# Optimization experiments

Measured on AMD Instinct MI355X. Metric: run time of the kernel, lower is better.

Reference implementation:

```python
import math
import jax, jax.numpy as jnp
import numpy as np

SCALE = 64.0
MARGIN = 0.5
T = 0.2
COS_M = math.cos(MARGIN)
SIN_M = math.sin(MARGIN)
TH = math.cos(math.pi - MARGIN)
MM = math.sin(math.pi - MARGIN) * MARGIN
EPS = 1e-07

B, D, C = 512, 512, 100000


def setup_inputs() -> dict:
    key = jax.random.key(0)
    k1, k2, k3 = jax.random.split(key, 3)
    embedding = jax.random.normal(k1, (B, D), dtype=jnp.float32)
    # xavier_uniform for (num_classes, embed_size)
    limit = math.sqrt(6.0 / (C + D))
    weight = jax.random.uniform(k2, (C, D), dtype=jnp.float32, minval=-limit, maxval=limit)
    ground_truth = jax.random.randint(k3, (B,), 0, C, dtype=jnp.int64)
    return {"embedding": embedding, "weight": weight, "ground_truth": ground_truth}


def reference(embedding, weight, ground_truth):
    gt = ground_truth.astype(jnp.int32)
    e = embedding / jnp.linalg.norm(embedding, axis=1, keepdims=True)
    w = weight / jnp.linalg.norm(weight, axis=1, keepdims=True)
    # (B, C) cosine similarities
    cos_theta = jnp.clip(jnp.einsum('bd,cd->bc', e, w), -1.0 + EPS, 1.0 - EPS)
    pos = jnp.take_along_axis(cos_theta, gt[:, None], axis=1)  # (B, 1)
    sin_theta = jnp.sqrt(jnp.clip(1.0 - pos * pos, EPS, 1.0 - EPS))
    phi = pos * COS_M - sin_theta * SIN_M
    phi = jnp.where(pos > TH, phi, pos - MM)  # easy_margin=False branch
    # hard-example reweighting: fixed=False -> (t+1)*cos + t where cos > phi
    mask = cos_theta > phi  # phi broadcasts (B,1) -> (B,C)
    cos_theta = jnp.where(mask, (T + 1.0) * cos_theta + T, cos_theta)
    # scatter phi into the ground-truth column
    output = cos_theta.at[jnp.arange(B), gt].set(phi[:, 0])
    output = output * SCALE
    # mean cross-entropy
    logp = jax.nn.log_softmax(output, axis=1)
    loss = -jnp.mean(jnp.take_along_axis(logp, gt[:, None], axis=1))
    return loss
```

## Files before the change

kernel.cpp:

```cpp
#include <hip/hip_runtime.h>
#include <hip/hip_bf16.h>
#include <stdint.h>

typedef unsigned short u16;
typedef __attribute__((ext_vector_type(8))) short short8;
typedef __attribute__((ext_vector_type(4))) float floatx4;

#define B_   512
#define D_   512
#define C_   100000

#define SCALE_  64.0f
#define COSM_   0.8775825618903728f
#define SINM_   0.479425538604203f
#define TH_     (-0.8775825618903728f)
#define MM_     0.2397127693021015f
#define EPS_    1e-7f
#define SHIFT_  89.6f

#define BM 256
#define BN 64
#define BK 32

__device__ inline float wave_reduce_sum(float v) {
    v += __shfl_xor(v, 1);
    v += __shfl_xor(v, 2);
    v += __shfl_xor(v, 4);
    v += __shfl_xor(v, 8);
    v += __shfl_xor(v, 16);
    v += __shfl_xor(v, 32);
    return v;
}

__device__ inline u16 f2bf(float x) {
    union { float f; uint32_t u; } v; v.f = x;
    uint32_t r = v.u + 0x7fffu + ((v.u >> 16) & 1u);
    return (u16)(r >> 16);
}

__global__ __launch_bounds__(256) void norm_e_phi_kernel(
    const float* __restrict__ emb, const float* __restrict__ w_raw,
    const int* __restrict__ gt, u16* __restrict__ e_bf16,
    float* __restrict__ phi, float* __restrict__ rowsum) {
    if (threadIdx.x < 4) rowsum[blockIdx.x * 4 + threadIdx.x] = 0.0f;
    int wv = threadIdx.x >> 6;
    int lane = threadIdx.x & 63;
    int b = blockIdx.x * 4 + wv;
    const float4* rp = (const float4*)(emb + (long)b * D_);
    float4 f0 = rp[lane], f1 = rp[lane + 64];
    float sq = f0.x*f0.x + f0.y*f0.y + f0.z*f0.z + f0.w*f0.w
             + f1.x*f1.x + f1.y*f1.y + f1.z*f1.z + f1.w*f1.w;
    sq = wave_reduce_sum(sq);
    float rn = 1.0f / sqrtf(sq);
    f0.x *= rn; f0.y *= rn; f0.z *= rn; f0.w *= rn;
    f1.x *= rn; f1.y *= rn; f1.z *= rn; f1.w *= rn;
    uint2 p0, p1;
    p0.x = (uint32_t)f2bf(f0.x) | ((uint32_t)f2bf(f0.y) << 16);
    p0.y = (uint32_t)f2bf(f0.z) | ((uint32_t)f2bf(f0.w) << 16);
    p1.x = (uint32_t)f2bf(f1.x) | ((uint32_t)f2bf(f1.y) << 16);
    p1.y = (uint32_t)f2bf(f1.z) | ((uint32_t)f2bf(f1.w) << 16);
    uint2* ob = (uint2*)(e_bf16 + (long)b * D_);
    ob[lane] = p0;
    ob[lane + 64] = p1;

    int g = gt[b];
    const float4* wp = (const float4*)(w_raw + (long)g * D_);
    float4 w0 = wp[lane], w1 = wp[lane + 64];
    float dt = f0.x*w0.x + f0.y*w0.y + f0.z*w0.z + f0.w*w0.w
             + f1.x*w1.x + f1.y*w1.y + f1.z*w1.z + f1.w*w1.w;
    float wsq = w0.x*w0.x + w0.y*w0.y + w0.z*w0.z + w0.w*w0.w
              + w1.x*w1.x + w1.y*w1.y + w1.z*w1.z + w1.w*w1.w;
    dt = wave_reduce_sum(dt);
    wsq = wave_reduce_sum(wsq);
    if (lane == 0) {
        float pos = dt / sqrtf(wsq);
        pos = fminf(fmaxf(pos, -1.0f + EPS_), 1.0f - EPS_);
        float s2 = 1.0f - pos * pos;
        s2 = fminf(fmaxf(s2, EPS_), 1.0f - EPS_);
        float sin_t = sqrtf(s2);
        float ph = pos * COSM_ - sin_t * SINM_;
        ph = (pos > TH_) ? ph : (pos - MM_);
        phi[b] = ph;
    }
}

__device__ inline void cvt_store(const float4& v0, const float4& v1,
                                 u16* dst, float& sq) {
    union { u16 h[8]; uint4 q; } u;
    u.h[0] = f2bf(v0.x); u.h[1] = f2bf(v0.y);
    u.h[2] = f2bf(v0.z); u.h[3] = f2bf(v0.w);
    u.h[4] = f2bf(v1.x); u.h[5] = f2bf(v1.y);
    u.h[6] = f2bf(v1.z); u.h[7] = f2bf(v1.w);
    *(uint4*)dst = u.q;
    sq += v0.x*v0.x + v0.y*v0.y + v0.z*v0.z + v0.w*v0.w
        + v1.x*v1.x + v1.y*v1.y + v1.z*v1.z + v1.w*v1.w;
}

__global__ __launch_bounds__(256, 3) void gemm_arcface_fused(
    const u16* __restrict__ a_g,
    const float* __restrict__ w_g,
    const float* __restrict__ phi, const int* __restrict__ gt,
    float* __restrict__ rowsum) {
    __shared__ __align__(16) u16 b_tile[2][BN * BK];
    __shared__ float phi_s[BM];
    __shared__ int gt_s[BM];
    __shared__ float rnorm_s[BN];

    int tid = threadIdx.x;
    int c0 = (blockIdx.x >> 1) * BN;
    int m0 = (blockIdx.x & 1) * BM;

    phi_s[tid] = phi[m0 + tid];
    gt_s[tid] = gt[m0 + tid];

    int rb = tid >> 2;
    int bslot = tid & 3;
    int bkq = bslot ^ ((rb >> 1) & 3);
    long brow_g = min(c0 + rb, C_ - 1);
    const float4* b_src = (const float4*)(w_g + brow_g * (long)D_ + bkq * 8);
    u16* b_dst0 = &b_tile[0][rb * BK + bslot * 8];
    u16* b_dst1 = &b_tile[1][rb * BK + bslot * 8];

    int wv = tid >> 6, lane = tid & 63;
    int low4 = lane & 15, quad = lane >> 4;
    int lslot = quad ^ ((low4 >> 1) & 3);
    const u16* a_base = a_g + (long)(m0 + wv * 64 + low4) * D_ + quad * 8;
    int bf_off = low4 * BK + lslot * 8;

    floatx4 acc[4][4] = {};
    float sq = 0.0f;
    float4 bv[2][2];
    short8 afc[4];

    bv[0][0] = b_src[0]; bv[0][1] = b_src[1];
    cvt_store(bv[0][0], bv[0][1], b_dst0, sq);
    bv[1][0] = b_src[8]; bv[1][1] = b_src[9];
    asm volatile("s_waitcnt lgkmcnt(0)" ::: "memory");
    __builtin_amdgcn_s_barrier();

#pragma unroll
    for (int kt = 0; kt < 16; kt++) {
        int p = kt & 1;
        if (kt < 14) {
            bv[p][0] = b_src[(kt + 2) * 8];
            bv[p][1] = b_src[(kt + 2) * 8 + 1];
        }
#pragma unroll
        for (int mi = 0; mi < 4; mi++)
            afc[mi] = *(const short8*)(a_base + (long)mi * 16 * D_ + kt * BK);
        short8 bf[4];
#pragma unroll
        for (int ni = 0; ni < 4; ni++)
            bf[ni] = *(const short8*)(&b_tile[p][ni * 16 * BK + bf_off]);
#pragma unroll
        for (int mi = 0; mi < 4; mi++)
#pragma unroll
            for (int ni = 0; ni < 4; ni++)
                acc[mi][ni] = __builtin_amdgcn_mfma_f32_16x16x32_bf16(
                    afc[mi], bf[ni], acc[mi][ni], 0, 0, 0);
        if (kt < 15)
            cvt_store(bv[1 - p][0], bv[1 - p][1], p ? b_dst0 : b_dst1, sq);
        asm volatile("s_waitcnt lgkmcnt(0)" ::: "memory");
        __builtin_amdgcn_s_barrier();
    }

    sq += __shfl_xor(sq, 1);
    sq += __shfl_xor(sq, 2);
    if ((tid & 3) == 0) rnorm_s[rb] = 1.0f / sqrtf(sq);
    __syncthreads();

#pragma unroll
    for (int mi = 0; mi < 4; mi++) {
#pragma unroll
        for (int r = 0; r < 4; r++) {
            int rl = wv * 64 + mi * 16 + quad * 4 + r;
            float ph = phi_s[rl];
            int g = gt_s[rl];
            float s = 0.0f;
#pragma unroll
            for (int ni = 0; ni < 4; ni++) {
                int cl = ni * 16 + low4;
                int c = c0 + cl;
                float v = acc[mi][ni][r] * rnorm_s[cl];
                v = fminf(fmaxf(v, -1.0f + EPS_), 1.0f - EPS_);
                float logit = (v > ph) ? (1.2f * v + 0.2f) : v;
                logit *= SCALE_;
                if (c == g) logit = SCALE_ * ph;
                s += (c < C_) ? __expf(logit - SHIFT_) : 0.0f;
            }
            s += __shfl_xor(s, 1);
            s += __shfl_xor(s, 2);
            s += __shfl_xor(s, 4);
            s += __shfl_xor(s, 8);
            if (low4 == 0) atomicAdd(&rowsum[m0 + rl], s);
        }
    }
}

__global__ __launch_bounds__(256) void loss_kernel(
    const float* __restrict__ rowsum, const float* __restrict__ phi,
    float* __restrict__ out) {
    __shared__ float red[4];
    int tid = threadIdx.x;
    float s = 0.0f;
    for (int b = tid; b < B_; b += 256)
        s += logf(rowsum[b]) + SHIFT_ - SCALE_ * phi[b];
    s = wave_reduce_sum(s);
    int wv = tid >> 6, lane = tid & 63;
    if (lane == 0) red[wv] = s;
    __syncthreads();
    if (tid == 0) out[0] = (red[0] + red[1] + red[2] + red[3]) * (1.0f / B_);
}

extern "C" void kernel_launch(void* const* d_in, const int* in_sizes, int n_in,
                              void* d_out, int out_size, void* d_ws, size_t ws_size,
                              hipStream_t stream) {
    const float* emb = (const float*)d_in[0];
    const float* wgt = (const float*)d_in[1];
    const int* gt = (const int*)d_in[2];
    float* out = (float*)d_out;

    char* ws = (char*)d_ws;
    u16* e_bf16 = (u16*)(ws);
    float* phi = (float*)(ws + 524288);
    float* rowsum = (float*)(ws + 526336);

    norm_e_phi_kernel<<<B_ / 4, 256, 0, stream>>>(emb, wgt, gt, e_bf16, phi, rowsum);
    int nc = (C_ + BN - 1) / BN;
    gemm_arcface_fused<<<nc * 2, 256, 0, stream>>>(e_bf16, wgt, phi, gt, rowsum);
    loss_kernel<<<1, 256, 0, stream>>>(rowsum, phi, out);
}
```

Measured before the change: 450.6 us.

## Halve class tile width, deepen weight prefetch, use packed bf16 conversion

Shrinks the class tile from 64 to 32 columns, so each block covers less of the weight matrix and the grid doubles. Each thread now loads one float4 per k-step with a four-deep register prefetch, and the hand-written bf16 rounding is replaced by the packed conversion intrinsic. Occupancy is raised to four blocks per SIMD. The C-bound guard is dropped because 100000 divides evenly by 32. The trade-off is that the A operand (the embedding fragments) is reread from global memory twice as often, since reuse per block falls.

```diff
diff --git a/kernel.cpp b/kernel.cpp
--- a/kernel.cpp
+++ b/kernel.cpp
@@ -19,7 +19,7 @@
 #define SHIFT_  89.6f
 
 #define BM 256
-#define BN 64
+#define BN 32
 #define BK 32
 
 __device__ inline float wave_reduce_sum(float v) {
@@ -36,6 +36,12 @@
     union { float f; uint32_t u; } v; v.f = x;
     uint32_t r = v.u + 0x7fffu + ((v.u >> 16) & 1u);
     return (u16)(r >> 16);
+}
+
+__device__ inline uint32_t cvt2_rn(float a, float b) {
+    union { __hip_bfloat162 h; uint32_t u; } v;
+    v.h = __float22bfloat162_rn(make_float2(a, b));
+    return v.u;
 }
 
 __global__ __launch_bounds__(256) void norm_e_phi_kernel(
@@ -84,19 +90,15 @@
     }
 }
 
-__device__ inline void cvt_store(const float4& v0, const float4& v1,
-                                 u16* dst, float& sq) {
-    union { u16 h[8]; uint4 q; } u;
-    u.h[0] = f2bf(v0.x); u.h[1] = f2bf(v0.y);
-    u.h[2] = f2bf(v0.z); u.h[3] = f2bf(v0.w);
-    u.h[4] = f2bf(v1.x); u.h[5] = f2bf(v1.y);
-    u.h[6] = f2bf(v1.z); u.h[7] = f2bf(v1.w);
-    *(uint4*)dst = u.q;
-    sq += v0.x*v0.x + v0.y*v0.y + v0.z*v0.z + v0.w*v0.w
-        + v1.x*v1.x + v1.y*v1.y + v1.z*v1.z + v1.w*v1.w;
-}
-
-__global__ __launch_bounds__(256, 3) void gemm_arcface_fused(
+__device__ inline void cvt_store1(const float4& v, u16* dst, float& sq) {
+    uint2 u;
+    u.x = cvt2_rn(v.x, v.y);
+    u.y = cvt2_rn(v.z, v.w);
+    *(uint2*)dst = u;
+    sq += v.x*v.x + v.y*v.y + v.z*v.z + v.w*v.w;
+}
+
+__global__ __launch_bounds__(256, 4) void gemm_arcface_fused(
     const u16* __restrict__ a_g,
     const float* __restrict__ w_g,
     const float* __restrict__ phi, const int* __restrict__ gt,
@@ -113,60 +115,57 @@
     phi_s[tid] = phi[m0 + tid];
     gt_s[tid] = gt[m0 + tid];
 
-    int rb = tid >> 2;
-    int bslot = tid & 3;
-    int bkq = bslot ^ ((rb >> 1) & 3);
-    long brow_g = min(c0 + rb, C_ - 1);
-    const float4* b_src = (const float4*)(w_g + brow_g * (long)D_ + bkq * 8);
-    u16* b_dst0 = &b_tile[0][rb * BK + bslot * 8];
-    u16* b_dst1 = &b_tile[1][rb * BK + bslot * 8];
+    int rb = tid >> 3;
+    int ls = tid & 7;
+    int key = (rb >> 1) & 3;
+    int pslot = (((ls >> 1) ^ key) << 1) | (ls & 1);
+    const float4* b_src = (const float4*)(w_g + (long)(c0 + rb) * D_) + ls;
+    u16* bd0 = &b_tile[0][rb * BK + pslot * 4];
+    u16* bd1 = &b_tile[1][rb * BK + pslot * 4];
 
     int wv = tid >> 6, lane = tid & 63;
     int low4 = lane & 15, quad = lane >> 4;
-    int lslot = quad ^ ((low4 >> 1) & 3);
     const u16* a_base = a_g + (long)(m0 + wv * 64 + low4) * D_ + quad * 8;
-    int bf_off = low4 * BK + lslot * 8;
-
-    floatx4 acc[4][4] = {};
+    int bf_off = low4 * BK + (quad ^ ((low4 >> 1) & 3)) * 8;
+
+    floatx4 acc[4][2] = {};
     float sq = 0.0f;
-    float4 bv[2][2];
-    short8 afc[4];
-
-    bv[0][0] = b_src[0]; bv[0][1] = b_src[1];
-    cvt_store(bv[0][0], bv[0][1], b_dst0, sq);
-    bv[1][0] = b_src[8]; bv[1][1] = b_src[9];
+    float4 bv[4];
+    short8 af[4];
+
+#pragma unroll
+    for (int j = 0; j < 4; j++) bv[j] = b_src[j * 8];
+    cvt_store1(bv[0], bd0, sq);
     asm volatile("s_waitcnt lgkmcnt(0)" ::: "memory");
     __builtin_amdgcn_s_barrier();
 
 #pragma unroll
     for (int kt = 0; kt < 16; kt++) {
         int p = kt & 1;
-        if (kt < 14) {
-            bv[p][0] = b_src[(kt + 2) * 8];
-            bv[p][1] = b_src[(kt + 2) * 8 + 1];
-        }
+        if (kt < 12) bv[kt & 3] = b_src[(kt + 4) * 8];
 #pragma unroll
         for (int mi = 0; mi < 4; mi++)
-            afc[mi] = *(const short8*)(a_base + (long)mi * 16 * D_ + kt * BK);
-        short8 bf[4];
-#pragma unroll
-        for (int ni = 0; ni < 4; ni++)
+            af[mi] = *(const short8*)(a_base + (long)mi * 16 * D_ + kt * BK);
+        short8 bf[2];
+#pragma unroll
+        for (int ni = 0; ni < 2; ni++)
             bf[ni] = *(const short8*)(&b_tile[p][ni * 16 * BK + bf_off]);
 #pragma unroll
         for (int mi = 0; mi < 4; mi++)
 #pragma unroll
-            for (int ni = 0; ni < 4; ni++)
+            for (int ni = 0; ni < 2; ni++)
                 acc[mi][ni] = __builtin_amdgcn_mfma_f32_16x16x32_bf16(
-                    afc[mi], bf[ni], acc[mi][ni], 0, 0, 0);
+                    af[mi], bf[ni], acc[mi][ni], 0, 0, 0);
         if (kt < 15)
-            cvt_store(bv[1 - p][0], bv[1 - p][1], p ? b_dst0 : b_dst1, sq);
+            cvt_store1(bv[(kt + 1) & 3], p ? bd0 : bd1, sq);
         asm volatile("s_waitcnt lgkmcnt(0)" ::: "memory");
         __builtin_amdgcn_s_barrier();
     }
 
     sq += __shfl_xor(sq, 1);
     sq += __shfl_xor(sq, 2);
-    if ((tid & 3) == 0) rnorm_s[rb] = 1.0f / sqrtf(sq);
+    sq += __shfl_xor(sq, 4);
+    if ((tid & 7) == 0) rnorm_s[rb] = 1.0f / sqrtf(sq);
     __syncthreads();
 
 #pragma unroll
@@ -178,7 +177,7 @@
             int g = gt_s[rl];
             float s = 0.0f;
 #pragma unroll
-            for (int ni = 0; ni < 4; ni++) {
+            for (int ni = 0; ni < 2; ni++) {
                 int cl = ni * 16 + low4;
                 int c = c0 + cl;
                 float v = acc[mi][ni][r] * rnorm_s[cl];
@@ -186,7 +185,7 @@
                 float logit = (v > ph) ? (1.2f * v + 0.2f) : v;
                 logit *= SCALE_;
                 if (c == g) logit = SCALE_ * ph;
-                s += (c < C_) ? __expf(logit - SHIFT_) : 0.0f;
+                s += __expf(logit - SHIFT_);
             }
             s += __shfl_xor(s, 1);
             s += __shfl_xor(s, 2);
@@ -226,7 +225,7 @@
     float* rowsum = (float*)(ws + 526336);
 
     norm_e_phi_kernel<<<B_ / 4, 256, 0, stream>>>(emb, wgt, gt, e_bf16, phi, rowsum);
-    int nc = (C_ + BN - 1) / BN;
+    int nc = C_ / BN;
     gemm_arcface_fused<<<nc * 2, 256, 0, stream>>>(e_bf16, wgt, phi, gt, rowsum);
     loss_kernel<<<1, 256, 0, stream>>>(rowsum, phi, out);
 }
```

Measured after the change: 580.3 us. 28.8% more time.
